# Kernel tuning notes

Hardware: AMD Instinct MI355X
Metric: run time of the kernel (lower is better)

Reference implementation:

```python
import jax, jax.numpy as jnp
import numpy as np

N = 50000
E = 800000
D_IN, D_HID, D_OUT = 128, 128, 64


def _glorot(key, shape):
    fan_in, fan_out = shape[1], shape[0]
    lim = np.sqrt(6.0 / (fan_in + fan_out))
    return jax.random.uniform(key, shape, jnp.float32, -lim, lim)


def setup_inputs() -> dict:
    key = jax.random.key(0)
    ks = jax.random.split(key, 12)
    x = jax.random.normal(ks[0], (N, D_IN), jnp.float32)
    edge_index = jax.random.randint(ks[1], (2, E), 0, N, jnp.int32)
    edge_attr = jax.random.uniform(ks[2], (E,), jnp.float32)
    return {
        "x": x,
        "edge_index": edge_index,
        "edge_attr": edge_attr,
        # conv1: in -> hidden
        "W1_rel": _glorot(ks[3], (D_HID, D_IN)),
        "b1_rel": jnp.zeros((D_HID,), jnp.float32),
        "W1_root": _glorot(ks[4], (D_HID, D_IN)),
        # conv_mu: hidden -> out
        "Wmu_rel": _glorot(ks[5], (D_OUT, D_HID)),
        "bmu_rel": jnp.zeros((D_OUT,), jnp.float32),
        "Wmu_root": _glorot(ks[6], (D_OUT, D_HID)),
        # conv_logvar: hidden -> out
        "Wlv_rel": _glorot(ks[7], (D_OUT, D_HID)),
        "blv_rel": jnp.zeros((D_OUT,), jnp.float32),
        "Wlv_root": _glorot(ks[8], (D_OUT, D_HID)),
    }


def sage_conv(x, src, dst, ew, W_rel, b_rel, W_root, n_nodes):
    # message: edge_weight * x_j  (gather from source nodes)
    msg = x[src] * ew[:, None]                                   # [E, d]
    agg = jax.ops.segment_sum(msg, dst, num_segments=n_nodes)    # [N, d]
    cnt = jax.ops.segment_sum(jnp.ones_like(ew), dst, num_segments=n_nodes)
    mean = agg / jnp.maximum(cnt, 1.0)[:, None]                  # scatter-mean
    return mean @ W_rel.T + b_rel + x @ W_root.T


def reference(x, edge_index, edge_attr, W1_rel, b1_rel, W1_root,
              Wmu_rel, bmu_rel, Wmu_root, Wlv_rel, blv_rel, Wlv_root):
    src, dst = edge_index[0], edge_index[1]
    h = jax.nn.elu(sage_conv(x, src, dst, edge_attr, W1_rel, b1_rel, W1_root, N))
    mu = sage_conv(h, src, dst, edge_attr, Wmu_rel, bmu_rel, Wmu_root, N)
    logvar = sage_conv(h, src, dst, edge_attr, Wlv_rel, blv_rel, Wlv_root, N)
    return mu, logvar
```

## Files before the change

kernel.cpp:

```cpp
#include <hip/hip_runtime.h>
#include <hip/hip_bf16.h>
#include <math.h>

#define NNODES 50000
#define NEDGES 800000
#define NRANGE 6250
#define NC     64
#define CHUNK_E (NEDGES / NC)
#define NSLICE 4
#define SLICE_E (CHUNK_E / NSLICE)

using short8 = __attribute__((ext_vector_type(8))) short;
using f32x4  = __attribute__((ext_vector_type(4))) float;
typedef unsigned long long u64;

__device__ __forceinline__ short f2bf(float f) {
    __hip_bfloat16 h = __float2bfloat16(f);
    return *reinterpret_cast<short*>(&h);
}


__global__ __launch_bounds__(512)
void prep_kernel(const float* __restrict__ x, __hip_bfloat16* __restrict__ xb,
                 const float* __restrict__ w0, const float* __restrict__ w1,
                 const float* __restrict__ w2, const float* __restrict__ w3,
                 const float* __restrict__ w4, const float* __restrict__ w5,
                 __hip_bfloat16* __restrict__ Wb,
                 const int* __restrict__ dst, unsigned int* __restrict__ partial,
                 unsigned char* __restrict__ rank8) {
    __shared__ unsigned int hist[NNODES / 4];
    int b = blockIdx.x;
    int tid = threadIdx.x;
    if (b < 64) {
        int c = b;
        for (int i = tid; i < NNODES / 4; i += 512) hist[i] = 0;
        __syncthreads();
        int base = c * CHUNK_E;
        for (int e = base + tid; e < base + CHUNK_E; e += 512) {
            int d = dst[e];
            int sh = 8 * (d & 3);
            unsigned int old = atomicAdd(&hist[d >> 2], 1u << sh);
            rank8[e] = (unsigned char)((old >> sh) & 0xffu);
        }
        __syncthreads();
        unsigned int* outp = partial + (size_t)c * (NNODES / 4);
        for (int i = tid; i < NNODES / 4; i += 512) outp[i] = hist[i];
    } else if (b < 1627) {
        int i = (b - 64) * 512 + tid;
        if (i < 800000) {
            const float4* p = (const float4*)x + (size_t)i * 2;
            float4 a = p[0], c4 = p[1];
            short8 o;
            o[0] = f2bf(a.x); o[1] = f2bf(a.y); o[2] = f2bf(a.z); o[3] = f2bf(a.w);
            o[4] = f2bf(c4.x); o[5] = f2bf(c4.y); o[6] = f2bf(c4.z); o[7] = f2bf(c4.w);
            *reinterpret_cast<short8*>((short*)xb + (size_t)i * 8) = o;
        }
    } else {
        int i = (b - 1627) * 512 + tid;
        const float* src; int off;
        if      (i < 16384) { src = w0; off = 0; }
        else if (i < 32768) { src = w1; off = 16384; }
        else if (i < 40960) { src = w2; off = 32768; }
        else if (i < 49152) { src = w3; off = 40960; }
        else if (i < 57344) { src = w4; off = 49152; }
        else                { src = w5; off = 57344; }
        Wb[i] = __float2bfloat16(src[i - off]);
    }
}


__global__ __launch_bounds__(1024)
void scan1_kernel(const unsigned int* __restrict__ partial,
                  unsigned char* __restrict__ cbase,
                  int* __restrict__ excl, int* __restrict__ bsum) {
    __shared__ int sdata[1024];
    int tid = threadIdx.x;
    int n = blockIdx.x * 1024 + tid;
    int deg = 0;
    if (n < NNODES) {
        int sh = 8 * (n & 3);
        int idx = n >> 2;
        unsigned int packed = 0;
        unsigned int* cbout = (unsigned int*)(cbase + (size_t)n * NC);
#pragma unroll 4
        for (int c = 0; c < NC; ++c) {
            unsigned int w = partial[(size_t)c * (NNODES / 4) + idx];
            unsigned int cc = (w >> sh) & 0xffu;
            packed |= ((unsigned int)(deg & 0xff)) << (8 * (c & 3));
            deg += (int)cc;
            if ((c & 3) == 3) { cbout[c >> 2] = packed; packed = 0; }
        }
    }
    sdata[tid] = deg;
    __syncthreads();
    for (int off = 1; off < 1024; off <<= 1) {
        int t = (tid >= off) ? sdata[tid - off] : 0;
        __syncthreads();
        sdata[tid] += t;
        __syncthreads();
    }
    if (n < NNODES) excl[n] = sdata[tid] - deg;
    if (tid == 1023) bsum[blockIdx.x] = sdata[1023];
}

__global__ __launch_bounds__(64)
void scan2_kernel(int* __restrict__ bsum, int nb) {
    int lane = threadIdx.x;
    int v = (lane < nb) ? bsum[lane] : 0;
    int incl = v;
    for (int off = 1; off < 64; off <<= 1) {
        int t = __shfl_up(incl, off);
        if (lane >= off) incl += t;
    }
    if (lane < nb) bsum[lane] = incl - v;
    if (lane == 63) bsum[nb] = incl;
}


__global__ __launch_bounds__(256)
void fill_kernel(const int* __restrict__ src, const int* __restrict__ dst,
                 const float* __restrict__ ew,
                 const int* __restrict__ excl, const int* __restrict__ bsum,
                 const unsigned char* __restrict__ cbase,
                 const unsigned char* __restrict__ rank8,
                 u64* __restrict__ edges) {
    int b = blockIdx.x;
    int r = b & 7;
    int t = b >> 3;
    int c = t & (NC - 1);
    int s = t >> 6;
    int lo = r * NRANGE;
    int base = c * CHUNK_E + s * SLICE_E;
    int end = base + SLICE_E;
    for (int e = base + threadIdx.x; e < end; e += 256) {
        int d = dst[e];
        unsigned int dl = (unsigned int)(d - lo);
        if (dl < NRANGE) {
            int slot = excl[d] + bsum[d >> 10] + (int)cbase[(size_t)d * NC + c] + (int)rank8[e];
            u64 pack = ((u64)(unsigned int)__float_as_int(ew[e]) << 32) | (unsigned int)src[e];
            edges[slot] = pack;
        }
    }
}


__device__ __forceinline__ void gstep(u64 e, const unsigned int* __restrict__ Fb,
                                      int lane, float& ax, float& ay) {
    unsigned int v = Fb[(size_t)(unsigned int)e * 64 + lane];
    float w = __uint_as_float((unsigned int)(e >> 32));
    ax += __uint_as_float(v << 16) * w;
    ay += __uint_as_float(v & 0xffff0000u) * w;
}

__device__ __forceinline__ unsigned int gather_node(const unsigned int* __restrict__ Fb,
                                                    const u64* __restrict__ edges,
                                                    int beg, int end, int lane) {
    float ax[8], ay[8];
#pragma unroll
    for (int j = 0; j < 8; ++j) { ax[j] = 0.f; ay[j] = 0.f; }
    int s = beg;
    for (; s + 8 <= end; s += 8) {
        u64 e[8];
#pragma unroll
        for (int j = 0; j < 8; ++j) e[j] = __builtin_nontemporal_load(edges + s + j);
#pragma unroll
        for (int j = 0; j < 8; ++j) gstep(e[j], Fb, lane, ax[j], ay[j]);
    }
    if (s + 4 <= end) {
        u64 e[4];
#pragma unroll
        for (int j = 0; j < 4; ++j) e[j] = __builtin_nontemporal_load(edges + s + j);
#pragma unroll
        for (int j = 0; j < 4; ++j) gstep(e[j], Fb, lane, ax[j], ay[j]);
        s += 4;
    }
    if (s + 2 <= end) {
        u64 e0 = __builtin_nontemporal_load(edges + s);
        u64 e1 = __builtin_nontemporal_load(edges + s + 1);
        gstep(e0, Fb, lane, ax[0], ay[0]);
        gstep(e1, Fb, lane, ax[1], ay[1]);
        s += 2;
    }
    if (s < end) {
        u64 e0 = __builtin_nontemporal_load(edges + s);
        gstep(e0, Fb, lane, ax[0], ay[0]);
    }
#pragma unroll
    for (int j = 4; j < 8; ++j) { ax[j - 4] += ax[j]; ay[j - 4] += ay[j]; }
    float axs = (ax[0] + ax[1]) + (ax[2] + ax[3]);
    float ays = (ay[0] + ay[1]) + (ay[2] + ay[3]);
    float inv = 1.f / fmaxf((float)(end - beg), 1.f);
    unsigned int lo = (unsigned int)(unsigned short)f2bf(axs * inv);
    unsigned int hi = (unsigned int)(unsigned short)f2bf(ays * inv);
    return lo | (hi << 16);
}


#define SMW 20

__global__ __launch_bounds__(256)
void fused1_kernel(const unsigned int* __restrict__ Fb,
                   const __hip_bfloat16* __restrict__ xb,
                   const int* __restrict__ excl, const int* __restrict__ bsum,
                   const u64* __restrict__ edges,
                   const __hip_bfloat16* __restrict__ Wb,
                   const float* __restrict__ bias,
                   __hip_bfloat16* __restrict__ outb,
                   int E) {
    __shared__ unsigned int smean[4][16][SMW];
    int wid  = threadIdx.x >> 6;
    int lane = threadIdx.x & 63;
    int nodeBase = blockIdx.x * 16;

    for (int q = 0; q < 4; ++q) {
        int nodeLocal = wid * 4 + q;
        int node = nodeBase + nodeLocal;
        int beg = excl[node] + bsum[node >> 10];
        int end = (node + 1 < NNODES) ? (excl[node + 1] + bsum[(node + 1) >> 10]) : E;
        beg = __builtin_amdgcn_readfirstlane(beg);
        end = __builtin_amdgcn_readfirstlane(end);
        unsigned int mv = gather_node(Fb, edges, beg, end, lane);
        smean[lane >> 4][nodeLocal][lane & 15] = mv;
    }
    __syncthreads();

    int m  = lane & 15;
    int kq = lane >> 4;
    short8 a1[4], a2[4];
    const short* A2p = (const short*)xb + (size_t)(nodeBase + m) * 128 + kq * 8;
#pragma unroll
    for (int kk = 0; kk < 4; ++kk) {
        a1[kk] = *(const short8*)((const short*)&smean[kk][m][kq * 4]);
        a2[kk] = *(const short8*)(A2p + kk * 32);
    }
    const short* Wrel  = (const short*)Wb;
    const short* Wroot = (const short*)Wb + 16384;

#pragma unroll
    for (int cc = 0; cc < 2; ++cc) {
        int c = wid * 2 + cc;
        f32x4 acc = {0.f, 0.f, 0.f, 0.f};
        const short* b1p = Wrel  + (size_t)(c * 16 + m) * 128 + kq * 8;
        const short* b2p = Wroot + (size_t)(c * 16 + m) * 128 + kq * 8;
#pragma unroll
        for (int kk = 0; kk < 4; ++kk) {
            short8 bw1 = *(const short8*)(b1p + kk * 32);
            acc = __builtin_amdgcn_mfma_f32_16x16x32_bf16(a1[kk], bw1, acc, 0, 0, 0);
            short8 bw2 = *(const short8*)(b2p + kk * 32);
            acc = __builtin_amdgcn_mfma_f32_16x16x32_bf16(a2[kk], bw2, acc, 0, 0, 0);
        }
        int col = c * 16 + m;
        float b = bias[col];
#pragma unroll
        for (int i = 0; i < 4; ++i) {
            int gn = nodeBase + kq * 4 + i;
            float v = acc[i] + b;
            v = (v > 0.f) ? v : expm1f(v);
            outb[(size_t)gn * 128 + col] = __float2bfloat16(v);
        }
    }
}

__global__ __launch_bounds__(256)
void fused2_kernel(const unsigned int* __restrict__ Fb,
                   const __hip_bfloat16* __restrict__ hb,
                   const int* __restrict__ excl, const int* __restrict__ bsum,
                   const u64* __restrict__ edges,
                   const __hip_bfloat16* __restrict__ Wb,
                   const float* __restrict__ bmu, const float* __restrict__ blv,
                   float* __restrict__ out,
                   int E) {
    __shared__ unsigned int smean[4][16][SMW];
    int wid  = threadIdx.x >> 6;
    int lane = threadIdx.x & 63;
    int nodeBase = blockIdx.x * 16;

    for (int q = 0; q < 4; ++q) {
        int nodeLocal = wid * 4 + q;
        int node = nodeBase + nodeLocal;
        int beg = excl[node] + bsum[node >> 10];
        int end = (node + 1 < NNODES) ? (excl[node + 1] + bsum[(node + 1) >> 10]) : E;
        beg = __builtin_amdgcn_readfirstlane(beg);
        end = __builtin_amdgcn_readfirstlane(end);
        unsigned int mv = gather_node(Fb, edges, beg, end, lane);
        smean[lane >> 4][nodeLocal][lane & 15] = mv;
    }
    __syncthreads();

    int m  = lane & 15;
    int kq = lane >> 4;
    short8 a1[4], a2[4];
    const short* A2p = (const short*)hb + (size_t)(nodeBase + m) * 128 + kq * 8;
#pragma unroll
    for (int kk = 0; kk < 4; ++kk) {
        a1[kk] = *(const short8*)((const short*)&smean[kk][m][kq * 4]);
        a2[kk] = *(const short8*)(A2p + kk * 32);
    }
    const short* WmuR = (const short*)Wb + 32768;
    const short* WmuT = (const short*)Wb + 40960;
    const short* WlvR = (const short*)Wb + 49152;
    const short* WlvT = (const short*)Wb + 57344;

    int c = wid;
    f32x4 accMu = {0.f, 0.f, 0.f, 0.f};
    f32x4 accLv = {0.f, 0.f, 0.f, 0.f};
    size_t wrow = (size_t)(c * 16 + m) * 128 + kq * 8;
#pragma unroll
    for (int kk = 0; kk < 4; ++kk) {
        short8 bm1 = *(const short8*)(WmuR + wrow + kk * 32);
        accMu = __builtin_amdgcn_mfma_f32_16x16x32_bf16(a1[kk], bm1, accMu, 0, 0, 0);
        short8 bm2 = *(const short8*)(WmuT + wrow + kk * 32);
        accMu = __builtin_amdgcn_mfma_f32_16x16x32_bf16(a2[kk], bm2, accMu, 0, 0, 0);
        short8 bl1 = *(const short8*)(WlvR + wrow + kk * 32);
        accLv = __builtin_amdgcn_mfma_f32_16x16x32_bf16(a1[kk], bl1, accLv, 0, 0, 0);
        short8 bl2 = *(const short8*)(WlvT + wrow + kk * 32);
        accLv = __builtin_amdgcn_mfma_f32_16x16x32_bf16(a2[kk], bl2, accLv, 0, 0, 0);
    }
    int col = c * 16 + m;
    float bmv = bmu[col], blv_ = blv[col];
#pragma unroll
    for (int i = 0; i < 4; ++i) {
        int gn = nodeBase + kq * 4 + i;
        out[(size_t)gn * 64 + col] = accMu[i] + bmv;
        out[(size_t)NNODES * 64 + (size_t)gn * 64 + col] = accLv[i] + blv_;
    }
}

extern "C" void kernel_launch(void* const* d_in, const int* in_sizes, int n_in,
                              void* d_out, int out_size, void* d_ws, size_t ws_size,
                              hipStream_t stream) {
    const float* x        = (const float*)d_in[0];
    const int*   eidx     = (const int*)d_in[1];
    const float* eattr    = (const float*)d_in[2];
    const float* W1_rel   = (const float*)d_in[3];
    const float* b1_rel   = (const float*)d_in[4];
    const float* W1_root  = (const float*)d_in[5];
    const float* Wmu_rel  = (const float*)d_in[6];
    const float* bmu_rel  = (const float*)d_in[7];
    const float* Wmu_root = (const float*)d_in[8];
    const float* Wlv_rel  = (const float*)d_in[9];
    const float* blv_rel  = (const float*)d_in[10];
    const float* Wlv_root = (const float*)d_in[11];
    float* out = (float*)d_out;

    const int N = NNODES, E = NEDGES;
    const int nb = (N + 1023) / 1024;
    const int* src = eidx;
    const int* dst = eidx + E;

    char* ws = (char*)d_ws;
    size_t off = 0;
    int* excl = (int*)(ws + off); off += (size_t)N * 4;
    int* bsum = (int*)(ws + off); off += 256;
    off = (off + 63) & ~(size_t)63;
    unsigned int* partial = (unsigned int*)(ws + off); off += (size_t)NC * (N / 4) * 4;
    unsigned char* cbase  = (unsigned char*)(ws + off); off += (size_t)N * NC;
    unsigned char* rank8  = (unsigned char*)(ws + off); off += (size_t)E;
    off = (off + 63) & ~(size_t)63;
    u64* edges = (u64*)(ws + off); off += (size_t)E * 8;
    __hip_bfloat16* xb    = (__hip_bfloat16*)(ws + off); off += (size_t)N * 128 * 2;
    __hip_bfloat16* hb    = (__hip_bfloat16*)(ws + off); off += (size_t)N * 128 * 2;
    __hip_bfloat16* Wb    = (__hip_bfloat16*)(ws + off); off += 65536 * 2;

    prep_kernel<<<1755, 512, 0, stream>>>(x, xb, W1_rel, W1_root, Wmu_rel, Wmu_root,
                                          Wlv_rel, Wlv_root, Wb, dst, partial, rank8);
    scan1_kernel<<<nb, 1024, 0, stream>>>(partial, cbase, excl, bsum);
    scan2_kernel<<<1, 64, 0, stream>>>(bsum, nb);
    fill_kernel<<<NC * 8 * NSLICE, 256, 0, stream>>>(src, dst, eattr, excl, bsum,
                                                     cbase, rank8, edges);

    fused1_kernel<<<N / 16, 256, 0, stream>>>(
        (const unsigned int*)xb, xb, excl, bsum, edges, Wb, b1_rel, hb, E);
    fused2_kernel<<<N / 16, 256, 0, stream>>>(
        (const unsigned int*)hb, hb, excl, bsum, edges, Wb, bmu_rel, blv_rel, out, E);
}
```

Before: 180.3 us.

## Transpose chunk-base table and halve fused-kernel block size with early root-operand loads

```diff
diff --git a/kernel.cpp b/kernel.cpp
--- a/kernel.cpp
+++ b/kernel.cpp
@@ -71,7 +71,7 @@
 
 __global__ __launch_bounds__(1024)
 void scan1_kernel(const unsigned int* __restrict__ partial,
-                  unsigned char* __restrict__ cbase,
+                  unsigned int* __restrict__ cbase4,
                   int* __restrict__ excl, int* __restrict__ bsum) {
     __shared__ int sdata[1024];
     int tid = threadIdx.x;
@@ -81,14 +81,13 @@
         int sh = 8 * (n & 3);
         int idx = n >> 2;
         unsigned int packed = 0;
-        unsigned int* cbout = (unsigned int*)(cbase + (size_t)n * NC);
 #pragma unroll 4
         for (int c = 0; c < NC; ++c) {
             unsigned int w = partial[(size_t)c * (NNODES / 4) + idx];
             unsigned int cc = (w >> sh) & 0xffu;
             packed |= ((unsigned int)(deg & 0xff)) << (8 * (c & 3));
             deg += (int)cc;
-            if ((c & 3) == 3) { cbout[c >> 2] = packed; packed = 0; }
+            if ((c & 3) == 3) { cbase4[(size_t)(c >> 2) * NNODES + n] = packed; packed = 0; }
         }
     }
     sdata[tid] = deg;
@@ -121,7 +120,7 @@
 void fill_kernel(const int* __restrict__ src, const int* __restrict__ dst,
                  const float* __restrict__ ew,
                  const int* __restrict__ excl, const int* __restrict__ bsum,
-                 const unsigned char* __restrict__ cbase,
+                 const unsigned int* __restrict__ cbase4,
                  const unsigned char* __restrict__ rank8,
                  u64* __restrict__ edges) {
     int b = blockIdx.x;
@@ -132,11 +131,14 @@
     int lo = r * NRANGE;
     int base = c * CHUNK_E + s * SLICE_E;
     int end = base + SLICE_E;
+    const unsigned int* cb = cbase4 + (size_t)(c >> 2) * NNODES;
+    int csh = 8 * (c & 3);
     for (int e = base + threadIdx.x; e < end; e += 256) {
         int d = dst[e];
         unsigned int dl = (unsigned int)(d - lo);
         if (dl < NRANGE) {
-            int slot = excl[d] + bsum[d >> 10] + (int)cbase[(size_t)d * NC + c] + (int)rank8[e];
+            int cbv = (int)((cb[d] >> csh) & 0xffu);
+            int slot = excl[d] + bsum[d >> 10] + cbv + (int)rank8[e];
             u64 pack = ((u64)(unsigned int)__float_as_int(ew[e]) << 32) | (unsigned int)src[e];
             edges[slot] = pack;
         }
@@ -198,7 +200,7 @@
 
 #define SMW 20
 
-__global__ __launch_bounds__(256)
+__global__ __launch_bounds__(128)
 void fused1_kernel(const unsigned int* __restrict__ Fb,
                    const __hip_bfloat16* __restrict__ xb,
                    const int* __restrict__ excl, const int* __restrict__ bsum,
@@ -211,9 +213,16 @@
     int wid  = threadIdx.x >> 6;
     int lane = threadIdx.x & 63;
     int nodeBase = blockIdx.x * 16;
-
-    for (int q = 0; q < 4; ++q) {
-        int nodeLocal = wid * 4 + q;
+    int m  = lane & 15;
+    int kq = lane >> 4;
+
+    short8 a2[4];
+    const short* A2p = (const short*)xb + (size_t)(nodeBase + m) * 128 + kq * 8;
+#pragma unroll
+    for (int kk = 0; kk < 4; ++kk) a2[kk] = *(const short8*)(A2p + kk * 32);
+
+    for (int q = 0; q < 8; ++q) {
+        int nodeLocal = wid * 8 + q;
         int node = nodeBase + nodeLocal;
         int beg = excl[node] + bsum[node >> 10];
         int end = (node + 1 < NNODES) ? (excl[node + 1] + bsum[(node + 1) >> 10]) : E;
@@ -224,21 +233,16 @@
     }
     __syncthreads();
 
-    int m  = lane & 15;
-    int kq = lane >> 4;
-    short8 a1[4], a2[4];
-    const short* A2p = (const short*)xb + (size_t)(nodeBase + m) * 128 + kq * 8;
-#pragma unroll
-    for (int kk = 0; kk < 4; ++kk) {
+    short8 a1[4];
+#pragma unroll
+    for (int kk = 0; kk < 4; ++kk)
         a1[kk] = *(const short8*)((const short*)&smean[kk][m][kq * 4]);
-        a2[kk] = *(const short8*)(A2p + kk * 32);
-    }
     const short* Wrel  = (const short*)Wb;
     const short* Wroot = (const short*)Wb + 16384;
 
 #pragma unroll
-    for (int cc = 0; cc < 2; ++cc) {
-        int c = wid * 2 + cc;
+    for (int cc = 0; cc < 4; ++cc) {
+        int c = wid * 4 + cc;
         f32x4 acc = {0.f, 0.f, 0.f, 0.f};
         const short* b1p = Wrel  + (size_t)(c * 16 + m) * 128 + kq * 8;
         const short* b2p = Wroot + (size_t)(c * 16 + m) * 128 + kq * 8;
@@ -261,7 +265,7 @@
     }
 }
 
-__global__ __launch_bounds__(256)
+__global__ __launch_bounds__(128)
 void fused2_kernel(const unsigned int* __restrict__ Fb,
                    const __hip_bfloat16* __restrict__ hb,
                    const int* __restrict__ excl, const int* __restrict__ bsum,
@@ -274,9 +278,16 @@
     int wid  = threadIdx.x >> 6;
     int lane = threadIdx.x & 63;
     int nodeBase = blockIdx.x * 16;
-
-    for (int q = 0; q < 4; ++q) {
-        int nodeLocal = wid * 4 + q;
+    int m  = lane & 15;
+    int kq = lane >> 4;
+
+    short8 a2[4];
+    const short* A2p = (const short*)hb + (size_t)(nodeBase + m) * 128 + kq * 8;
+#pragma unroll
+    for (int kk = 0; kk < 4; ++kk) a2[kk] = *(const short8*)(A2p + kk * 32);
+
+    for (int q = 0; q < 8; ++q) {
+        int nodeLocal = wid * 8 + q;
         int node = nodeBase + nodeLocal;
         int beg = excl[node] + bsum[node >> 10];
         int end = (node + 1 < NNODES) ? (excl[node + 1] + bsum[(node + 1) >> 10]) : E;
@@ -287,42 +298,40 @@
     }
     __syncthreads();
 
-    int m  = lane & 15;
-    int kq = lane >> 4;
-    short8 a1[4], a2[4];
-    const short* A2p = (const short*)hb + (size_t)(nodeBase + m) * 128 + kq * 8;
-#pragma unroll
-    for (int kk = 0; kk < 4; ++kk) {
+    short8 a1[4];
+#pragma unroll
+    for (int kk = 0; kk < 4; ++kk)
         a1[kk] = *(const short8*)((const short*)&smean[kk][m][kq * 4]);
-        a2[kk] = *(const short8*)(A2p + kk * 32);
-    }
     const short* WmuR = (const short*)Wb + 32768;
     const short* WmuT = (const short*)Wb + 40960;
     const short* WlvR = (const short*)Wb + 49152;
     const short* WlvT = (const short*)Wb + 57344;
 
-    int c = wid;
-    f32x4 accMu = {0.f, 0.f, 0.f, 0.f};
-    f32x4 accLv = {0.f, 0.f, 0.f, 0.f};
-    size_t wrow = (size_t)(c * 16 + m) * 128 + kq * 8;
-#pragma unroll
-    for (int kk = 0; kk < 4; ++kk) {
-        short8 bm1 = *(const short8*)(WmuR + wrow + kk * 32);
-        accMu = __builtin_amdgcn_mfma_f32_16x16x32_bf16(a1[kk], bm1, accMu, 0, 0, 0);
-        short8 bm2 = *(const short8*)(WmuT + wrow + kk * 32);
-        accMu = __builtin_amdgcn_mfma_f32_16x16x32_bf16(a2[kk], bm2, accMu, 0, 0, 0);
-        short8 bl1 = *(const short8*)(WlvR + wrow + kk * 32);
-        accLv = __builtin_amdgcn_mfma_f32_16x16x32_bf16(a1[kk], bl1, accLv, 0, 0, 0);
-        short8 bl2 = *(const short8*)(WlvT + wrow + kk * 32);
-        accLv = __builtin_amdgcn_mfma_f32_16x16x32_bf16(a2[kk], bl2, accLv, 0, 0, 0);
-    }
-    int col = c * 16 + m;
-    float bmv = bmu[col], blv_ = blv[col];
-#pragma unroll
-    for (int i = 0; i < 4; ++i) {
-        int gn = nodeBase + kq * 4 + i;
-        out[(size_t)gn * 64 + col] = accMu[i] + bmv;
-        out[(size_t)NNODES * 64 + (size_t)gn * 64 + col] = accLv[i] + blv_;
+#pragma unroll
+    for (int cc = 0; cc < 2; ++cc) {
+        int c = wid * 2 + cc;
+        f32x4 accMu = {0.f, 0.f, 0.f, 0.f};
+        f32x4 accLv = {0.f, 0.f, 0.f, 0.f};
+        size_t wrow = (size_t)(c * 16 + m) * 128 + kq * 8;
+#pragma unroll
+        for (int kk = 0; kk < 4; ++kk) {
+            short8 bm1 = *(const short8*)(WmuR + wrow + kk * 32);
+            accMu = __builtin_amdgcn_mfma_f32_16x16x32_bf16(a1[kk], bm1, accMu, 0, 0, 0);
+            short8 bm2 = *(const short8*)(WmuT + wrow + kk * 32);
+            accMu = __builtin_amdgcn_mfma_f32_16x16x32_bf16(a2[kk], bm2, accMu, 0, 0, 0);
+            short8 bl1 = *(const short8*)(WlvR + wrow + kk * 32);
+            accLv = __builtin_amdgcn_mfma_f32_16x16x32_bf16(a1[kk], bl1, accLv, 0, 0, 0);
+            short8 bl2 = *(const short8*)(WlvT + wrow + kk * 32);
+            accLv = __builtin_amdgcn_mfma_f32_16x16x32_bf16(a2[kk], bl2, accLv, 0, 0, 0);
+        }
+        int col = c * 16 + m;
+        float bmv = bmu[col], blv_ = blv[col];
+#pragma unroll
+        for (int i = 0; i < 4; ++i) {
+            int gn = nodeBase + kq * 4 + i;
+            out[(size_t)gn * 64 + col] = accMu[i] + bmv;
+            out[(size_t)NNODES * 64 + (size_t)gn * 64 + col] = accLv[i] + blv_;
+        }
     }
 }
 
@@ -354,7 +363,7 @@
     int* bsum = (int*)(ws + off); off += 256;
     off = (off + 63) & ~(size_t)63;
     unsigned int* partial = (unsigned int*)(ws + off); off += (size_t)NC * (N / 4) * 4;
-    unsigned char* cbase  = (unsigned char*)(ws + off); off += (size_t)N * NC;
+    unsigned int* cbase4  = (unsigned int*)(ws + off); off += (size_t)16 * N * 4;
     unsigned char* rank8  = (unsigned char*)(ws + off); off += (size_t)E;
     off = (off + 63) & ~(size_t)63;
     u64* edges = (u64*)(ws + off); off += (size_t)E * 8;
@@ -364,13 +373,13 @@
 
     prep_kernel<<<1755, 512, 0, stream>>>(x, xb, W1_rel, W1_root, Wmu_rel, Wmu_root,
                                           Wlv_rel, Wlv_root, Wb, dst, partial, rank8);
-    scan1_kernel<<<nb, 1024, 0, stream>>>(partial, cbase, excl, bsum);
+    scan1_kernel<<<nb, 1024, 0, stream>>>(partial, cbase4, excl, bsum);
     scan2_kernel<<<1, 64, 0, stream>>>(bsum, nb);
     fill_kernel<<<NC * 8 * NSLICE, 256, 0, stream>>>(src, dst, eattr, excl, bsum,
-                                                     cbase, rank8, edges);
-
-    fused1_kernel<<<N / 16, 256, 0, stream>>>(
+                                                     cbase4, rank8, edges);
+
+    fused1_kernel<<<N / 16, 128, 0, stream>>>(
         (const unsigned int*)xb, xb, excl, bsum, edges, Wb, b1_rel, hb, E);
-    fused2_kernel<<<N / 16, 256, 0, stream>>>(
+    fused2_kernel<<<N / 16, 128, 0, stream>>>(
         (const unsigned int*)hb, hb, excl, bsum, edges, Wb, bmu_rel, blv_rel, out, E);
 }
```

Measured after the change: 186.9 us. 1.04x slower.
